# Performance work log

Hardware: AMD Instinct MI355X
Metric: run time of the kernel (lower is better)

## Reference

```python
import jax, jax.numpy as jnp
import numpy as np


def _cubic(x):
    absx = np.abs(x)
    absx2 = absx ** 2
    absx3 = absx ** 3
    return ((1.5 * absx3 - 2.5 * absx2 + 1) * (absx <= 1)
            + (-0.5 * absx3 + 2.5 * absx2 - 4 * absx + 2) * ((1 < absx) & (absx <= 2)))


def _contributions(in_length, out_length, scale):
    # Replicates Resizer.contributions for cubic kernel with antialiasing (scale < 1).
    kernel_width = 4.0 / scale
    fixed_kernel = lambda arg: scale * _cubic(scale * arg)
    out_coordinates = np.arange(1, out_length + 1)
    shifted = out_coordinates - (out_length - in_length * scale) / 2
    match = shifted / scale + 0.5 * (1 - 1 / scale)
    left = np.floor(match - kernel_width / 2)
    expanded = int(np.ceil(kernel_width) + 2)
    fov = np.int16(left[:, None] + np.arange(expanded) - 1)  # (out, taps)
    weights = fixed_kernel(1.0 * match[:, None] - fov - 1)
    s = np.sum(weights, axis=1)
    s[s == 0] = 1.0
    weights = weights / s[:, None]
    mirror = np.concatenate((np.arange(in_length), np.arange(in_length - 1, -1, -1)))
    fov = mirror[np.mod(fov, mirror.shape[0])]
    nz = np.nonzero(np.any(weights, axis=0))[0]  # drop all-zero taps
    return weights[:, nz], fov[:, nz]


IN_SHAPE = (32, 3, 512, 512)
OUT_HW = 256
SCALE = 0.5
NDIM_TRAIL = 3  # len(scale_factor) - 1 trailing singleton dims on weights


def setup_inputs() -> dict:
    key = jax.random.key(0)
    in_tensor = jax.random.normal(key, IN_SHAPE, dtype=jnp.float32)
    w_np, fov_np = _contributions(IN_SHAPE[2], OUT_HW, SCALE)
    taps, out_len = w_np.shape[1], w_np.shape[0]
    w = jnp.asarray(w_np.T.reshape((taps, out_len) + (1,) * NDIM_TRAIL), dtype=jnp.float32)
    fov = jnp.asarray(fov_np.T, dtype=jnp.int32)  # (taps, out)
    # H and W have identical in/out lengths and scale -> identical tables
    return {"in_tensor": in_tensor, "w2": w, "fov2": fov, "w3": w, "fov3": fov}


def reference(in_tensor, w2, fov2, w3, fov3):
    x = in_tensor
    for dim, fov, w in ((2, fov2, w2), (3, fov3, w3)):
        x = jnp.swapaxes(x, dim, 0)          # bring resized axis to front
        x = jnp.sum(x[fov] * w, axis=0)      # gather (taps,out,...) * w -> (out,...)
        x = jnp.swapaxes(x, dim, 0)
    return x
```

## Files before the change

kernel.cpp:

```cpp
#include <hip/hip_runtime.h>


#define H_IN   512
#define W_IN   512
#define H_OUT  256
#define W_OUT  256
#define BC     96
#define TAPS   8
#define OHC    16
#define OWC    8

__device__ __forceinline__ int mir(int r, int n) {
    r = (r < 0) ? (-1 - r) : r;
    r = (r >= n) ? (2 * n - 1 - r) : r;
    return r;
}

__global__ __launch_bounds__(256) void pass1(const float* __restrict__ in,
                                             const float* __restrict__ wt,
                                             float* __restrict__ mid) {
    int g   = blockIdx.x * 256 + threadIdx.x;
    int w4  = g & 127;
    int ohc = (g >> 7) & 15;
    int bc  = g >> 11;

    int oh0 = ohc * OHC;

    float K[TAPS];
#pragma unroll
    for (int i = 0; i < TAPS; ++i) K[i] = wt[i * H_OUT];

    const float4* src = (const float4*)(in + (size_t)bc * H_IN * W_IN) + w4;

    float4 acc[OHC];
#pragma unroll
    for (int k = 0; k < OHC; ++k) acc[k] = make_float4(0.f, 0.f, 0.f, 0.f);

    const int rbase = 2 * oh0 - 3;
#pragma unroll
    for (int rr = 0; rr < 2 * OHC + 6; ++rr) {
        int rm = mir(rbase + rr, H_IN);
        float4 x = src[(size_t)rm * (W_IN / 4)];
#pragma unroll
        for (int k = 0; k < OHC; ++k) {
            int i = rr - 2 * k;
            if (0 <= i && i < TAPS) {
                float kw = K[i];
                acc[k].x += kw * x.x;
                acc[k].y += kw * x.y;
                acc[k].z += kw * x.z;
                acc[k].w += kw * x.w;
            }
        }
    }

    float4* dst = (float4*)(mid + (size_t)bc * H_OUT * W_IN) + w4;
#pragma unroll
    for (int k = 0; k < OHC; ++k)
        dst[(size_t)(oh0 + k) * (W_IN / 4)] = acc[k];
}

__global__ __launch_bounds__(256) void pass2(const float* __restrict__ mid,
                                             const float* __restrict__ wt,
                                             float* __restrict__ out) {
    int g   = blockIdx.x * 256 + threadIdx.x;
    int owc = g & 31;
    int oh  = (g >> 5) & 255;
    int bc  = g >> 13;

    int ow0 = owc * OWC;

    float K[TAPS];
#pragma unroll
    for (int i = 0; i < TAPS; ++i) K[i] = wt[i * W_OUT];

    const float* src = mid + ((size_t)bc * H_OUT + oh) * W_IN;

    float win[2 * OWC + 6];
    const int cbase = 2 * ow0 - 3;
#pragma unroll
    for (int t = 0; t < 2 * OWC + 6; ++t)
        win[t] = src[mir(cbase + t, W_IN)];

    float res[OWC];
#pragma unroll
    for (int k = 0; k < OWC; ++k) {
        float s = 0.f;
#pragma unroll
        for (int j = 0; j < TAPS; ++j)
            s += K[j] * win[2 * k + j];
        res[k] = s;
    }

    float* dstrow = out + ((size_t)bc * H_OUT + oh) * W_OUT + ow0;
    float4* dv = (float4*)dstrow;
    dv[0] = make_float4(res[0], res[1], res[2], res[3]);
    dv[1] = make_float4(res[4], res[5], res[6], res[7]);
}

__global__ __launch_bounds__(256) void fused(const float* __restrict__ in,
                                             const float* __restrict__ wt,
                                             float* __restrict__ out) {
    int g = blockIdx.x * 256 + threadIdx.x;
    if (g >= BC * H_OUT * W_OUT) return;
    int ow = g & 255;
    int oh = (g >> 8) & 255;
    int bc = g >> 16;

    float K[TAPS];
#pragma unroll
    for (int i = 0; i < TAPS; ++i) K[i] = wt[i * H_OUT];

    float s = 0.f;
#pragma unroll
    for (int i = 0; i < TAPS; ++i) {
        const float* row =
            in + ((size_t)bc * H_IN + mir(2 * oh + i - 3, H_IN)) * W_IN;
        float t = 0.f;
#pragma unroll
        for (int j = 0; j < TAPS; ++j)
            t += K[j] * row[mir(2 * ow + j - 3, W_IN)];
        s += K[i] * t;
    }
    out[g] = s;
}

extern "C" void kernel_launch(void* const* d_in, const int* in_sizes, int n_in,
                              void* d_out, int out_size, void* d_ws, size_t ws_size,
                              hipStream_t stream) {
    const float* in = (const float*)d_in[0];
    const float* w2 = (const float*)d_in[1];
    const float* w3 = (const float*)d_in[3];
    float* out = (float*)d_out;

    const size_t mid_bytes = (size_t)BC * H_OUT * W_IN * sizeof(float);

    if (ws_size >= mid_bytes) {
        float* mid = (float*)d_ws;
        pass1<<<(BC * 16 * 128) / 256, 256, 0, stream>>>(in, w2, mid);
        pass2<<<(BC * 256 * 32) / 256, 256, 0, stream>>>(mid, w3, out);
    } else {
        fused<<<(BC * H_OUT * W_OUT + 255) / 256, 256, 0, stream>>>(in, w2, out);
    }
}
```

Measured before the change: 180.7 us.

## Fuse vertical and horizontal resize passes via shared-memory tile

Replaces the two-pass scheme, which wrote a full intermediate buffer to global memory and read it back, with a single fused kernel. Each block first filters 22 input rows vertically into an 8x262 shared-memory tile, then filters that tile horizontally to produce 8x128 outputs. This removes the intermediate global round trip and one launch. The cost is halo recomputation (22 rows read per 8 output rows, extra columns at tile edges) and scalar rather than float4 loads. It also drops the w3 table and reuses w2, relying on the two tables being identical.

```diff
diff --git a/kernel.cpp b/kernel.cpp
--- a/kernel.cpp
+++ b/kernel.cpp
@@ -7,8 +7,10 @@
 #define W_OUT  256
 #define BC     96
 #define TAPS   8
-#define OHC    16
-#define OWC    8
+#define OH_T   8
+#define OW_T   128
+#define IN_ROWS (2 * OH_T + 6)
+#define MID_COLS (2 * OW_T + 6)
 
 __device__ __forceinline__ int mir(int r, int n) {
     r = (r < 0) ? (-1 - r) : r;
@@ -16,113 +18,61 @@
     return r;
 }
 
-__global__ __launch_bounds__(256) void pass1(const float* __restrict__ in,
-                                             const float* __restrict__ wt,
-                                             float* __restrict__ mid) {
-    int g   = blockIdx.x * 256 + threadIdx.x;
-    int w4  = g & 127;
-    int ohc = (g >> 7) & 15;
-    int bc  = g >> 11;
+__global__ __launch_bounds__(256) void resize_fused(const float* __restrict__ in,
+                                                    const float* __restrict__ wt,
+                                                    float* __restrict__ out) {
+    __shared__ float mid[OH_T][MID_COLS];
 
-    int oh0 = ohc * OHC;
+    const int bid = blockIdx.x;
+    const int owt = bid & 1;
+    const int oht = (bid >> 1) & 31;
+    const int bc  = bid >> 6;
+    const int oh0 = oht * OH_T;
+    const int ow0 = owt * OW_T;
+    const int t   = threadIdx.x;
 
     float K[TAPS];
 #pragma unroll
     for (int i = 0; i < TAPS; ++i) K[i] = wt[i * H_OUT];
 
-    const float4* src = (const float4*)(in + (size_t)bc * H_IN * W_IN) + w4;
+    const float* src = in + (size_t)bc * H_IN * W_IN;
+    const int rbase = 2 * oh0 - 3;
+    const int cbase = 2 * ow0 - 3;
 
-    float4 acc[OHC];
+    for (int c = t; c < MID_COLS; c += 256) {
+        const int gc = mir(cbase + c, W_IN);
+        float acc[OH_T];
 #pragma unroll
-    for (int k = 0; k < OHC; ++k) acc[k] = make_float4(0.f, 0.f, 0.f, 0.f);
+        for (int k = 0; k < OH_T; ++k) acc[k] = 0.f;
 
-    const int rbase = 2 * oh0 - 3;
 #pragma unroll
-    for (int rr = 0; rr < 2 * OHC + 6; ++rr) {
-        int rm = mir(rbase + rr, H_IN);
-        float4 x = src[(size_t)rm * (W_IN / 4)];
+        for (int r = 0; r < IN_ROWS; ++r) {
+            const float x = src[(size_t)mir(rbase + r, H_IN) * W_IN + gc];
 #pragma unroll
-        for (int k = 0; k < OHC; ++k) {
-            int i = rr - 2 * k;
-            if (0 <= i && i < TAPS) {
-                float kw = K[i];
-                acc[k].x += kw * x.x;
-                acc[k].y += kw * x.y;
-                acc[k].z += kw * x.z;
-                acc[k].w += kw * x.w;
+            for (int k = 0; k < OH_T; ++k) {
+                const int i = r - 2 * k;
+                if (0 <= i && i < TAPS) acc[k] += K[i] * x;
             }
         }
+#pragma unroll
+        for (int k = 0; k < OH_T; ++k) mid[k][c] = acc[k];
     }
 
-    float4* dst = (float4*)(mid + (size_t)bc * H_OUT * W_IN) + w4;
+    __syncthreads();
+
+    const int owl = t & (OW_T - 1);
+    const int r0  = (t >> 7) * 4;
+    float* dst = out + ((size_t)bc * H_OUT + oh0) * W_OUT + ow0 + owl;
+
 #pragma unroll
-    for (int k = 0; k < OHC; ++k)
-        dst[(size_t)(oh0 + k) * (W_IN / 4)] = acc[k];
-}
-
-__global__ __launch_bounds__(256) void pass2(const float* __restrict__ mid,
-                                             const float* __restrict__ wt,
-                                             float* __restrict__ out) {
-    int g   = blockIdx.x * 256 + threadIdx.x;
-    int owc = g & 31;
-    int oh  = (g >> 5) & 255;
-    int bc  = g >> 13;
-
-    int ow0 = owc * OWC;
-
-    float K[TAPS];
-#pragma unroll
-    for (int i = 0; i < TAPS; ++i) K[i] = wt[i * W_OUT];
-
-    const float* src = mid + ((size_t)bc * H_OUT + oh) * W_IN;
-
-    float win[2 * OWC + 6];
-    const int cbase = 2 * ow0 - 3;
-#pragma unroll
-    for (int t = 0; t < 2 * OWC + 6; ++t)
-        win[t] = src[mir(cbase + t, W_IN)];
-
-    float res[OWC];
-#pragma unroll
-    for (int k = 0; k < OWC; ++k) {
+    for (int rr = 0; rr < 4; ++rr) {
+        const int row = r0 + rr;
         float s = 0.f;
 #pragma unroll
         for (int j = 0; j < TAPS; ++j)
-            s += K[j] * win[2 * k + j];
-        res[k] = s;
+            s += K[j] * mid[row][2 * owl + j];
+        dst[(size_t)row * W_OUT] = s;
     }
-
-    float* dstrow = out + ((size_t)bc * H_OUT + oh) * W_OUT + ow0;
-    float4* dv = (float4*)dstrow;
-    dv[0] = make_float4(res[0], res[1], res[2], res[3]);
-    dv[1] = make_float4(res[4], res[5], res[6], res[7]);
-}
-
-__global__ __launch_bounds__(256) void fused(const float* __restrict__ in,
-                                             const float* __restrict__ wt,
-                                             float* __restrict__ out) {
-    int g = blockIdx.x * 256 + threadIdx.x;
-    if (g >= BC * H_OUT * W_OUT) return;
-    int ow = g & 255;
-    int oh = (g >> 8) & 255;
-    int bc = g >> 16;
-
-    float K[TAPS];
-#pragma unroll
-    for (int i = 0; i < TAPS; ++i) K[i] = wt[i * H_OUT];
-
-    float s = 0.f;
-#pragma unroll
-    for (int i = 0; i < TAPS; ++i) {
-        const float* row =
-            in + ((size_t)bc * H_IN + mir(2 * oh + i - 3, H_IN)) * W_IN;
-        float t = 0.f;
-#pragma unroll
-        for (int j = 0; j < TAPS; ++j)
-            t += K[j] * row[mir(2 * ow + j - 3, W_IN)];
-        s += K[i] * t;
-    }
-    out[g] = s;
 }
 
 extern "C" void kernel_launch(void* const* d_in, const int* in_sizes, int n_in,
@@ -130,16 +80,8 @@
                               hipStream_t stream) {
     const float* in = (const float*)d_in[0];
     const float* w2 = (const float*)d_in[1];
-    const float* w3 = (const float*)d_in[3];
     float* out = (float*)d_out;
+    (void)d_ws; (void)ws_size;
 
-    const size_t mid_bytes = (size_t)BC * H_OUT * W_IN * sizeof(float);
-
-    if (ws_size >= mid_bytes) {
-        float* mid = (float*)d_ws;
-        pass1<<<(BC * 16 * 128) / 256, 256, 0, stream>>>(in, w2, mid);
-        pass2<<<(BC * 256 * 32) / 256, 256, 0, stream>>>(mid, w3, out);
-    } else {
-        fused<<<(BC * H_OUT * W_OUT + 255) / 256, 256, 0, stream>>>(in, w2, out);
-    }
+    resize_fused<<<BC * 32 * 2, 256, 0, stream>>>(in, w2, out);
 }
```

Measured after the change: 158.5 us. -12.3%, faster.
